# Kernel optimization log

Measured on AMD Instinct MI355X. Metric: run time of the kernel, lower is better.

Reference implementation:

```python
import jax, jax.numpy as jnp
import numpy as np

BLOCK_SIZE = 256
EMB = 384
HEAD = 64
B = 256
T = 256

def setup_inputs() -> dict:
    key = jax.random.key(0)
    k1, k2, k3, k4 = jax.random.split(key, 4)
    x = jax.random.normal(k1, (B, T, EMB), dtype=jnp.float32)
    # torch Linear(no bias) default init ~ U(-1/sqrt(in), 1/sqrt(in)); use scaled normal
    s = 1.0 / np.sqrt(EMB)
    Wq = jax.random.normal(k2, (EMB, HEAD), dtype=jnp.float32) * s
    Wk = jax.random.normal(k3, (EMB, HEAD), dtype=jnp.float32) * s
    Wv = jax.random.normal(k4, (EMB, HEAD), dtype=jnp.float32) * s
    return {"x": x, "Wq": Wq, "Wk": Wk, "Wv": Wv}

def reference(x, Wq, Wk, Wv):
    Bb, Tt, C = x.shape
    q = jnp.einsum('btc,ch->bth', x, Wq)
    k = jnp.einsum('btc,ch->bth', x, Wk)
    v = jnp.einsum('btc,ch->bth', x, Wv)
    # NOTE: source scales by C**-0.5 where C = embedding dim (384), not head_size
    scores = jnp.einsum('bth,bsh->bts', q, k) * (C ** -0.5)  # [B,T,T]
    causal = jnp.tril(jnp.ones((Tt, Tt), dtype=bool))
    scores = jnp.where(causal, scores, -jnp.inf)
    weights = jax.nn.softmax(scores, axis=-1)
    # dropout is identity in eval mode (reference baseline)
    out = jnp.einsum('bts,bsh->bth', weights, v)
    return out
```

## Files before the change

kernel.cpp:

```cpp
#include <hip/hip_runtime.h>
#include <hip/hip_bf16.h>
#include <cstdint>
#include <cstddef>

#define B_DIM 256
#define T_DIM 256
#define EMB   384
#define HEAD  64

typedef __attribute__((ext_vector_type(8))) short bf16x8;
typedef __attribute__((ext_vector_type(4))) float f32x4;
typedef __attribute__((ext_vector_type(4))) unsigned int u32x4;

__device__ __forceinline__ unsigned short f2bf(float f) {
    union { float f; unsigned int u; } v; v.f = f;
    unsigned int r = v.u + 0x7fffu + ((v.u >> 16) & 1u);
    return (unsigned short)(r >> 16);
}

__device__ __forceinline__ unsigned int pkbf(float a, float b) {
#if __has_builtin(__builtin_amdgcn_cvt_pk_bf16_f32)
    typedef __attribute__((ext_vector_type(2))) __bf16 bf16x2_t;
    bf16x2_t r = __builtin_amdgcn_cvt_pk_bf16_f32(a, b);
    return *(unsigned int*)&r;
#else
    return (unsigned)f2bf(a) | ((unsigned)f2bf(b) << 16);
#endif
}

__global__ void wprep_kernel(const float* __restrict__ Wq, const float* __restrict__ Wk,
                             const float* __restrict__ Wv, unsigned short* __restrict__ Wb) {
    int g = blockIdx.x * blockDim.x + threadIdx.x;
    if (g >= 9216) return;
    int kkstep = g / 1536, rem = g - kkstep * 1536;
    int r = rem >> 3, cs = rem & 7, c = cs ^ (r & 7);
    const float* W = (r < 64) ? Wq : (r < 128) ? Wk : Wv;
    int h = r & 63;
    unsigned short tmp[8];
#pragma unroll
    for (int e = 0; e < 8; ++e) {
        int k = kkstep * 64 + c * 8 + e;
        tmp[e] = f2bf(W[k * HEAD + h]);
    }
    *(u32x4*)(Wb + (size_t)g * 8) = *(u32x4*)tmp;
}

__global__ __launch_bounds__(512, 1) void fused_kernel(const float* __restrict__ x,
                                                       const unsigned short* __restrict__ Wb,
                                                       float* __restrict__ out) {
    __shared__ union SM {
        struct { unsigned short Xst[6][128][64]; unsigned short Ws[2][12288]; } p1;
        struct { unsigned short qs[256][72]; unsigned short ks[256][72];
                 unsigned short vT[64][264]; unsigned short Ps[8][16][72]; } p2;
    } sm;

    const int tid = threadIdx.x;
    const int w = tid >> 6, lane = tid & 63, qd = lane >> 4, l15 = lane & 15;
    const int wm = w >> 2, wn = w & 3;
    const int b = blockIdx.x;
    const float* xb = x + (size_t)b * T_DIM * EMB;
    const int trow = tid >> 4, fc = tid & 15;

#define WGLDS(KSTEP, BUF) do { \
    _Pragma("unroll") \
    for (int s = 0; s < 3; ++s) { \
        int idx = s * 512 + w * 64; \
        const unsigned short* gp = Wb + (size_t)((KSTEP) * 1536 + idx + lane) * 8; \
        unsigned short* lp = &sm.p1.Ws[BUF][idx * 8]; \
        __builtin_amdgcn_global_load_lds( \
            (const __attribute__((address_space(1))) unsigned int*)gp, \
            (__attribute__((address_space(3))) unsigned int*)lp, 16, 0, 0); \
    } \
} while (0)

#define XLOAD(P, RG) do { \
    _Pragma("unroll") \
    for (int kk = 0; kk < 6; ++kk) \
        xq[(RG) & 1][kk] = *(const float4*)(xb + (size_t)((P) * 128 + (RG) * 32 + trow) * EMB + kk * 64 + 4 * fc); \
} while (0)

#define XCW(RG) do { \
    int row_ = (RG) * 32 + trow; \
    _Pragma("unroll") \
    for (int kk = 0; kk < 6; ++kk) { \
        float4 v_ = xq[(RG) & 1][kk]; \
        *(uint2*)((char*)&sm.p1.Xst[kk][row_][0] + ((((fc >> 1) ^ (row_ & 7)) << 4) | ((fc & 1) << 3))) = \
            make_uint2(pkbf(v_.x, v_.y), pkbf(v_.z, v_.w)); \
    } \
} while (0)

    f32x4 acc[2][4][3];
#pragma unroll
    for (int P = 0; P < 2; ++P)
#pragma unroll
        for (int mt = 0; mt < 4; ++mt)
#pragma unroll
            for (int nt = 0; nt < 3; ++nt) acc[P][mt][nt] = (f32x4){0.f, 0.f, 0.f, 0.f};

    float4 xq[2][6];

#pragma unroll
    for (int P = 0; P < 2; ++P) {
        WGLDS(0, 0);
        XLOAD(P, 0); XLOAD(P, 1);
        XCW(0);
        XLOAD(P, 2);
        XCW(1);
        XLOAD(P, 3);
        XCW(2);
        XCW(3);

#pragma unroll
        for (int kk = 0; kk < 6; ++kk) {
            __syncthreads();
            if (kk < 5) WGLDS(kk + 1, (kk + 1) & 1);
#pragma unroll
            for (int kb = 0; kb < 2; ++kb) {
                bf16x8 a[4], bb[3];
#pragma unroll
                for (int mt = 0; mt < 4; ++mt) {
                    int rl = 64 * wm + 16 * mt + l15;
                    a[mt] = *(const bf16x8*)((const char*)&sm.p1.Xst[kk][rl][0] +
                                             ((((kb << 2) + qd) ^ (rl & 7)) << 4));
                }
#pragma unroll
                for (int nt = 0; nt < 3; ++nt) {
                    int n = 48 * wn + 16 * nt + l15;
                    bb[nt] = *(const bf16x8*)&sm.p1.Ws[kk & 1][n * 64 + (((4 * kb + qd) ^ (n & 7)) << 3)];
                }
#pragma unroll
                for (int mt = 0; mt < 4; ++mt)
#pragma unroll
                    for (int nt = 0; nt < 3; ++nt)
                        acc[P][mt][nt] = __builtin_amdgcn_mfma_f32_16x16x32_bf16(a[mt], bb[nt], acc[P][mt][nt], 0, 0, 0);
            }
        }
        __syncthreads();
    }

#pragma unroll
    for (int P = 0; P < 2; ++P)
#pragma unroll
        for (int nt = 0; nt < 3; ++nt) {
            int n = 48 * wn + 16 * nt + l15;
            int arr = n >> 6, hh = n & 63;
            if (arr == 2) {
#pragma unroll
                for (int mt = 0; mt < 4; ++mt) {
                    int tok0 = 128 * P + 64 * wm + 16 * mt + 4 * qd;
                    *(uint2*)&sm.p2.vT[hh][tok0] = make_uint2(
                        pkbf(acc[P][mt][nt][0], acc[P][mt][nt][1]),
                        pkbf(acc[P][mt][nt][2], acc[P][mt][nt][3]));
                }
            } else {
#pragma unroll
                for (int mt = 0; mt < 4; ++mt)
#pragma unroll
                    for (int reg = 0; reg < 4; ++reg) {
                        int tok = 128 * P + 64 * wm + 16 * mt + 4 * qd + reg;
                        unsigned short val = f2bf(acc[P][mt][nt][reg]);
                        if (arr == 0) sm.p2.qs[tok][hh] = val;
                        else          sm.p2.ks[tok][hh] = val;
                    }
            }
        }
    __syncthreads();

    const int tiles[2] = { w, 15 - w };
    bf16x8 aq[2][2];
#pragma unroll
    for (int ti = 0; ti < 2; ++ti)
#pragma unroll
        for (int kbi = 0; kbi < 2; ++kbi)
            aq[ti][kbi] = *(const bf16x8*)&sm.p2.qs[16 * tiles[ti] + l15][32 * kbi + 8 * qd];

    f32x4 O[2][4];
    float l[2][4];
#pragma unroll
    for (int ti = 0; ti < 2; ++ti) {
#pragma unroll
        for (int dn = 0; dn < 4; ++dn) O[ti][dn] = (f32x4){0.f, 0.f, 0.f, 0.f};
#pragma unroll
        for (int reg = 0; reg < 4; ++reg) l[ti][reg] = 0.f;
    }

    const float cExp = 1.4426950408889634f / 19.595917942265423f;

#pragma unroll
    for (int ti = 0; ti < 2; ++ti) {
        const int t = tiles[ti];
        for (int jc = 0; jc <= (t >> 2); ++jc) {
            const int ntmax = min(3, t - 4 * jc);
            f32x4 S[4];
#pragma unroll
            for (int nt = 0; nt < 4; ++nt) {
                if (nt <= ntmax) {
                    bf16x8 b0 = *(const bf16x8*)&sm.p2.ks[64 * jc + 16 * nt + l15][8 * qd];
                    bf16x8 b1 = *(const bf16x8*)&sm.p2.ks[64 * jc + 16 * nt + l15][32 + 8 * qd];
                    f32x4 s = __builtin_amdgcn_mfma_f32_16x16x32_bf16(aq[ti][0], b0, (f32x4){0.f,0.f,0.f,0.f}, 0, 0, 0);
                    s = __builtin_amdgcn_mfma_f32_16x16x32_bf16(aq[ti][1], b1, s, 0, 0, 0);
                    S[nt] = s;
                }
            }
#pragma unroll
            for (int nt = 0; nt < 4; ++nt) {
#pragma unroll
                for (int reg = 0; reg < 4; ++reg) {
                    float p = 0.0f;
                    if (nt <= ntmax) {
                        p = exp2f(S[nt][reg] * cExp);
                        if (4 * jc + nt == t && (l15 > 4 * qd + reg)) p = 0.0f;
                    }
                    l[ti][reg] += p;
                    sm.p2.Ps[w][4 * qd + reg][16 * nt + l15] = f2bf(p);
                }
            }
            bf16x8 ap0 = *(const bf16x8*)&sm.p2.Ps[w][l15][8 * qd];
            bf16x8 ap1 = *(const bf16x8*)&sm.p2.Ps[w][l15][32 + 8 * qd];
#pragma unroll
            for (int dn = 0; dn < 4; ++dn) {
                bf16x8 bv0 = *(const bf16x8*)&sm.p2.vT[16 * dn + l15][64 * jc + 8 * qd];
                bf16x8 bv1 = *(const bf16x8*)&sm.p2.vT[16 * dn + l15][64 * jc + 32 + 8 * qd];
                O[ti][dn] = __builtin_amdgcn_mfma_f32_16x16x32_bf16(ap0, bv0, O[ti][dn], 0, 0, 0);
                O[ti][dn] = __builtin_amdgcn_mfma_f32_16x16x32_bf16(ap1, bv1, O[ti][dn], 0, 0, 0);
            }
        }
    }

#pragma unroll
    for (int ti = 0; ti < 2; ++ti) {
#pragma unroll
        for (int reg = 0; reg < 4; ++reg) {
            float s = l[ti][reg];
            s += __shfl_xor(s, 1);
            s += __shfl_xor(s, 2);
            s += __shfl_xor(s, 4);
            s += __shfl_xor(s, 8);
            float inv = 1.0f / s;
            int row = 16 * tiles[ti] + 4 * qd + reg;
            float* dst = out + ((size_t)b * T_DIM + row) * HEAD;
#pragma unroll
            for (int dn = 0; dn < 4; ++dn)
                dst[16 * dn + l15] = O[ti][dn][reg] * inv;
        }
    }
}

extern "C" void kernel_launch(void* const* d_in, const int* in_sizes, int n_in,
                              void* d_out, int out_size, void* d_ws, size_t ws_size,
                              hipStream_t stream) {
    const float* x  = (const float*)d_in[0];
    const float* Wq = (const float*)d_in[1];
    const float* Wk = (const float*)d_in[2];
    const float* Wv = (const float*)d_in[3];
    float* out = (float*)d_out;

    unsigned short* Wb = (unsigned short*)d_ws;

    wprep_kernel<<<36, 256, 0, stream>>>(Wq, Wk, Wv, Wb);
    fused_kernel<<<B_DIM, 512, 0, stream>>>(x, Wb, out);
}
```

Baseline: 173.8 us.

## Double block to 1024 threads and stream x per k-step with double buffering

Raises the workgroup from 8 to 16 waves. The projection now covers all 256 tokens in one pass, with x loaded per 64-wide k-chunk into a double-buffered padded LDS tile and prefetched in registers across the MFMA loop. In the attention phase each wave owns one query tile instead of two, with tiles assigned so that long and short causal rows are spread across waves. This aims to raise latency hiding and parallelism per CU. In exchange, register budget per thread shrinks, there are more barriers per k-step, and the padded unswizzled x layout may cause LDS bank conflicts.

```diff
diff --git a/kernel.cpp b/kernel.cpp
--- a/kernel.cpp
+++ b/kernel.cpp
@@ -45,13 +45,13 @@
     *(u32x4*)(Wb + (size_t)g * 8) = *(u32x4*)tmp;
 }
 
-__global__ __launch_bounds__(512, 1) void fused_kernel(const float* __restrict__ x,
-                                                       const unsigned short* __restrict__ Wb,
-                                                       float* __restrict__ out) {
+__global__ __launch_bounds__(1024, 1) void fused_kernel(const float* __restrict__ x,
+                                                        const unsigned short* __restrict__ Wb,
+                                                        float* __restrict__ out) {
     __shared__ union SM {
-        struct { unsigned short Xst[6][128][64]; unsigned short Ws[2][12288]; } p1;
+        struct { unsigned short Xs[2][256][72]; unsigned short Ws[2][12288]; } p1;
         struct { unsigned short qs[256][72]; unsigned short ks[256][72];
-                 unsigned short vT[64][264]; unsigned short Ps[8][16][72]; } p2;
+                 unsigned short vT[64][264]; unsigned short Ps[16][16][72]; } p2;
     } sm;
 
     const int tid = threadIdx.x;
@@ -59,190 +59,167 @@
     const int wm = w >> 2, wn = w & 3;
     const int b = blockIdx.x;
     const float* xb = x + (size_t)b * T_DIM * EMB;
-    const int trow = tid >> 4, fc = tid & 15;
+    const int xrow = tid >> 2, xj = tid & 3;
 
 #define WGLDS(KSTEP, BUF) do { \
     _Pragma("unroll") \
-    for (int s = 0; s < 3; ++s) { \
-        int idx = s * 512 + w * 64; \
-        const unsigned short* gp = Wb + (size_t)((KSTEP) * 1536 + idx + lane) * 8; \
-        unsigned short* lp = &sm.p1.Ws[BUF][idx * 8]; \
-        __builtin_amdgcn_global_load_lds( \
-            (const __attribute__((address_space(1))) unsigned int*)gp, \
-            (__attribute__((address_space(3))) unsigned int*)lp, 16, 0, 0); \
+    for (int s = 0; s < 2; ++s) { \
+        int idx = s * 1024 + w * 64; \
+        if (idx < 1536) { \
+            const unsigned short* gp = Wb + (size_t)((KSTEP) * 1536 + idx + lane) * 8; \
+            unsigned short* lp = &sm.p1.Ws[BUF][idx * 8]; \
+            __builtin_amdgcn_global_load_lds( \
+                (const __attribute__((address_space(1))) unsigned int*)gp, \
+                (__attribute__((address_space(3))) unsigned int*)lp, 16, 0, 0); \
+        } \
     } \
 } while (0)
 
-#define XLOAD(P, RG) do { \
+#define XLOAD(KK) do { \
     _Pragma("unroll") \
-    for (int kk = 0; kk < 6; ++kk) \
-        xq[(RG) & 1][kk] = *(const float4*)(xb + (size_t)((P) * 128 + (RG) * 32 + trow) * EMB + kk * 64 + 4 * fc); \
+    for (int i = 0; i < 4; ++i) \
+        xr[i] = *(const float4*)(xb + (size_t)xrow * EMB + (KK) * 64 + (4 * xj + i) * 4); \
 } while (0)
 
-#define XCW(RG) do { \
-    int row_ = (RG) * 32 + trow; \
+#define XWRITE(BUF) do { \
     _Pragma("unroll") \
-    for (int kk = 0; kk < 6; ++kk) { \
-        float4 v_ = xq[(RG) & 1][kk]; \
-        *(uint2*)((char*)&sm.p1.Xst[kk][row_][0] + ((((fc >> 1) ^ (row_ & 7)) << 4) | ((fc & 1) << 3))) = \
-            make_uint2(pkbf(v_.x, v_.y), pkbf(v_.z, v_.w)); \
-    } \
+    for (int i = 0; i < 4; ++i) \
+        *(uint2*)&sm.p1.Xs[BUF][xrow][4 * (4 * xj + i)] = \
+            make_uint2(pkbf(xr[i].x, xr[i].y), pkbf(xr[i].z, xr[i].w)); \
 } while (0)
 
-    f32x4 acc[2][4][3];
-#pragma unroll
-    for (int P = 0; P < 2; ++P)
-#pragma unroll
-        for (int mt = 0; mt < 4; ++mt)
-#pragma unroll
-            for (int nt = 0; nt < 3; ++nt) acc[P][mt][nt] = (f32x4){0.f, 0.f, 0.f, 0.f};
-
-    float4 xq[2][6];
-
-#pragma unroll
-    for (int P = 0; P < 2; ++P) {
-        WGLDS(0, 0);
-        XLOAD(P, 0); XLOAD(P, 1);
-        XCW(0);
-        XLOAD(P, 2);
-        XCW(1);
-        XLOAD(P, 3);
-        XCW(2);
-        XCW(3);
-
-#pragma unroll
-        for (int kk = 0; kk < 6; ++kk) {
-            __syncthreads();
-            if (kk < 5) WGLDS(kk + 1, (kk + 1) & 1);
-#pragma unroll
-            for (int kb = 0; kb < 2; ++kb) {
-                bf16x8 a[4], bb[3];
-#pragma unroll
-                for (int mt = 0; mt < 4; ++mt) {
-                    int rl = 64 * wm + 16 * mt + l15;
-                    a[mt] = *(const bf16x8*)((const char*)&sm.p1.Xst[kk][rl][0] +
-                                             ((((kb << 2) + qd) ^ (rl & 7)) << 4));
+    float4 xr[4];
+    WGLDS(0, 0);
+    XLOAD(0);
+    XWRITE(0);
+
+    f32x4 acc[4][3];
+#pragma unroll
+    for (int mt = 0; mt < 4; ++mt)
+#pragma unroll
+        for (int nt = 0; nt < 3; ++nt) acc[mt][nt] = (f32x4){0.f, 0.f, 0.f, 0.f};
+
+#pragma unroll
+    for (int kk = 0; kk < 6; ++kk) {
+        __syncthreads();
+        if (kk < 5) {
+            WGLDS(kk + 1, (kk + 1) & 1);
+            XLOAD(kk + 1);
+        }
+#pragma unroll
+        for (int kb = 0; kb < 2; ++kb) {
+            bf16x8 a[4], bb[3];
+#pragma unroll
+            for (int mt = 0; mt < 4; ++mt)
+                a[mt] = *(const bf16x8*)&sm.p1.Xs[kk & 1][64 * wm + 16 * mt + l15][32 * kb + 8 * qd];
+#pragma unroll
+            for (int nt = 0; nt < 3; ++nt) {
+                int n = 48 * wn + 16 * nt + l15;
+                bb[nt] = *(const bf16x8*)&sm.p1.Ws[kk & 1][n * 64 + (((4 * kb + qd) ^ (n & 7)) << 3)];
+            }
+#pragma unroll
+            for (int mt = 0; mt < 4; ++mt)
+#pragma unroll
+                for (int nt = 0; nt < 3; ++nt)
+                    acc[mt][nt] = __builtin_amdgcn_mfma_f32_16x16x32_bf16(a[mt], bb[nt], acc[mt][nt], 0, 0, 0);
+        }
+        if (kk < 5) XWRITE((kk + 1) & 1);
+    }
+    __syncthreads();
+
+#pragma unroll
+    for (int nt = 0; nt < 3; ++nt) {
+        int n = 48 * wn + 16 * nt + l15;
+        int arr = n >> 6, hh = n & 63;
+        if (arr == 2) {
+#pragma unroll
+            for (int mt = 0; mt < 4; ++mt) {
+                int tok0 = 64 * wm + 16 * mt + 4 * qd;
+                *(uint2*)&sm.p2.vT[hh][tok0] = make_uint2(
+                    pkbf(acc[mt][nt][0], acc[mt][nt][1]),
+                    pkbf(acc[mt][nt][2], acc[mt][nt][3]));
+            }
+        } else {
+#pragma unroll
+            for (int mt = 0; mt < 4; ++mt)
+#pragma unroll
+                for (int reg = 0; reg < 4; ++reg) {
+                    int tok = 64 * wm + 16 * mt + 4 * qd + reg;
+                    unsigned short val = f2bf(acc[mt][nt][reg]);
+                    if (arr == 0) sm.p2.qs[tok][hh] = val;
+                    else          sm.p2.ks[tok][hh] = val;
                 }
-#pragma unroll
-                for (int nt = 0; nt < 3; ++nt) {
-                    int n = 48 * wn + 16 * nt + l15;
-                    bb[nt] = *(const bf16x8*)&sm.p1.Ws[kk & 1][n * 64 + (((4 * kb + qd) ^ (n & 7)) << 3)];
+        }
+    }
+    __syncthreads();
+
+    const int slot = w >> 2, sid = w & 3;
+    const int t = (slot < 2) ? (2 * sid + slot) : (15 - 2 * sid - (slot & 1));
+
+    bf16x8 aq[2];
+#pragma unroll
+    for (int kbi = 0; kbi < 2; ++kbi)
+        aq[kbi] = *(const bf16x8*)&sm.p2.qs[16 * t + l15][32 * kbi + 8 * qd];
+
+    f32x4 O[4];
+    float l[4];
+#pragma unroll
+    for (int dn = 0; dn < 4; ++dn) O[dn] = (f32x4){0.f, 0.f, 0.f, 0.f};
+#pragma unroll
+    for (int reg = 0; reg < 4; ++reg) l[reg] = 0.f;
+
+    const float cExp = 1.4426950408889634f / 19.595917942265423f;
+
+    for (int jc = 0; jc <= (t >> 2); ++jc) {
+        const int ntmax = min(3, t - 4 * jc);
+        f32x4 S[4];
+#pragma unroll
+        for (int nt = 0; nt < 4; ++nt) {
+            if (nt <= ntmax) {
+                bf16x8 b0 = *(const bf16x8*)&sm.p2.ks[64 * jc + 16 * nt + l15][8 * qd];
+                bf16x8 b1 = *(const bf16x8*)&sm.p2.ks[64 * jc + 16 * nt + l15][32 + 8 * qd];
+                f32x4 s = __builtin_amdgcn_mfma_f32_16x16x32_bf16(aq[0], b0, (f32x4){0.f,0.f,0.f,0.f}, 0, 0, 0);
+                s = __builtin_amdgcn_mfma_f32_16x16x32_bf16(aq[1], b1, s, 0, 0, 0);
+                S[nt] = s;
+            }
+        }
+#pragma unroll
+        for (int nt = 0; nt < 4; ++nt) {
+#pragma unroll
+            for (int reg = 0; reg < 4; ++reg) {
+                float p = 0.0f;
+                if (nt <= ntmax) {
+                    p = exp2f(S[nt][reg] * cExp);
+                    if (4 * jc + nt == t && (l15 > 4 * qd + reg)) p = 0.0f;
                 }
-#pragma unroll
-                for (int mt = 0; mt < 4; ++mt)
-#pragma unroll
-                    for (int nt = 0; nt < 3; ++nt)
-                        acc[P][mt][nt] = __builtin_amdgcn_mfma_f32_16x16x32_bf16(a[mt], bb[nt], acc[P][mt][nt], 0, 0, 0);
-            }
-        }
-        __syncthreads();
-    }
-
-#pragma unroll
-    for (int P = 0; P < 2; ++P)
-#pragma unroll
-        for (int nt = 0; nt < 3; ++nt) {
-            int n = 48 * wn + 16 * nt + l15;
-            int arr = n >> 6, hh = n & 63;
-            if (arr == 2) {
-#pragma unroll
-                for (int mt = 0; mt < 4; ++mt) {
-                    int tok0 = 128 * P + 64 * wm + 16 * mt + 4 * qd;
-                    *(uint2*)&sm.p2.vT[hh][tok0] = make_uint2(
-                        pkbf(acc[P][mt][nt][0], acc[P][mt][nt][1]),
-                        pkbf(acc[P][mt][nt][2], acc[P][mt][nt][3]));
-                }
-            } else {
-#pragma unroll
-                for (int mt = 0; mt < 4; ++mt)
-#pragma unroll
-                    for (int reg = 0; reg < 4; ++reg) {
-                        int tok = 128 * P + 64 * wm + 16 * mt + 4 * qd + reg;
-                        unsigned short val = f2bf(acc[P][mt][nt][reg]);
-                        if (arr == 0) sm.p2.qs[tok][hh] = val;
-                        else          sm.p2.ks[tok][hh] = val;
-                    }
-            }
-        }
-    __syncthreads();
-
-    const int tiles[2] = { w, 15 - w };
-    bf16x8 aq[2][2];
-#pragma unroll
-    for (int ti = 0; ti < 2; ++ti)
-#pragma unroll
-        for (int kbi = 0; kbi < 2; ++kbi)
-            aq[ti][kbi] = *(const bf16x8*)&sm.p2.qs[16 * tiles[ti] + l15][32 * kbi + 8 * qd];
-
-    f32x4 O[2][4];
-    float l[2][4];
-#pragma unroll
-    for (int ti = 0; ti < 2; ++ti) {
-#pragma unroll
-        for (int dn = 0; dn < 4; ++dn) O[ti][dn] = (f32x4){0.f, 0.f, 0.f, 0.f};
-#pragma unroll
-        for (int reg = 0; reg < 4; ++reg) l[ti][reg] = 0.f;
-    }
-
-    const float cExp = 1.4426950408889634f / 19.595917942265423f;
-
-#pragma unroll
-    for (int ti = 0; ti < 2; ++ti) {
-        const int t = tiles[ti];
-        for (int jc = 0; jc <= (t >> 2); ++jc) {
-            const int ntmax = min(3, t - 4 * jc);
-            f32x4 S[4];
-#pragma unroll
-            for (int nt = 0; nt < 4; ++nt) {
-                if (nt <= ntmax) {
-                    bf16x8 b0 = *(const bf16x8*)&sm.p2.ks[64 * jc + 16 * nt + l15][8 * qd];
-                    bf16x8 b1 = *(const bf16x8*)&sm.p2.ks[64 * jc + 16 * nt + l15][32 + 8 * qd];
-                    f32x4 s = __builtin_amdgcn_mfma_f32_16x16x32_bf16(aq[ti][0], b0, (f32x4){0.f,0.f,0.f,0.f}, 0, 0, 0);
-                    s = __builtin_amdgcn_mfma_f32_16x16x32_bf16(aq[ti][1], b1, s, 0, 0, 0);
-                    S[nt] = s;
-                }
-            }
-#pragma unroll
-            for (int nt = 0; nt < 4; ++nt) {
-#pragma unroll
-                for (int reg = 0; reg < 4; ++reg) {
-                    float p = 0.0f;
-                    if (nt <= ntmax) {
-                        p = exp2f(S[nt][reg] * cExp);
-                        if (4 * jc + nt == t && (l15 > 4 * qd + reg)) p = 0.0f;
-                    }
-                    l[ti][reg] += p;
-                    sm.p2.Ps[w][4 * qd + reg][16 * nt + l15] = f2bf(p);
-                }
-            }
-            bf16x8 ap0 = *(const bf16x8*)&sm.p2.Ps[w][l15][8 * qd];
-            bf16x8 ap1 = *(const bf16x8*)&sm.p2.Ps[w][l15][32 + 8 * qd];
-#pragma unroll
-            for (int dn = 0; dn < 4; ++dn) {
-                bf16x8 bv0 = *(const bf16x8*)&sm.p2.vT[16 * dn + l15][64 * jc + 8 * qd];
-                bf16x8 bv1 = *(const bf16x8*)&sm.p2.vT[16 * dn + l15][64 * jc + 32 + 8 * qd];
-                O[ti][dn] = __builtin_amdgcn_mfma_f32_16x16x32_bf16(ap0, bv0, O[ti][dn], 0, 0, 0);
-                O[ti][dn] = __builtin_amdgcn_mfma_f32_16x16x32_bf16(ap1, bv1, O[ti][dn], 0, 0, 0);
-            }
-        }
-    }
-
-#pragma unroll
-    for (int ti = 0; ti < 2; ++ti) {
-#pragma unroll
-        for (int reg = 0; reg < 4; ++reg) {
-            float s = l[ti][reg];
-            s += __shfl_xor(s, 1);
-            s += __shfl_xor(s, 2);
-            s += __shfl_xor(s, 4);
-            s += __shfl_xor(s, 8);
-            float inv = 1.0f / s;
-            int row = 16 * tiles[ti] + 4 * qd + reg;
-            float* dst = out + ((size_t)b * T_DIM + row) * HEAD;
-#pragma unroll
-            for (int dn = 0; dn < 4; ++dn)
-                dst[16 * dn + l15] = O[ti][dn][reg] * inv;
-        }
+                l[reg] += p;
+                sm.p2.Ps[w][4 * qd + reg][16 * nt + l15] = f2bf(p);
+            }
+        }
+        bf16x8 ap0 = *(const bf16x8*)&sm.p2.Ps[w][l15][8 * qd];
+        bf16x8 ap1 = *(const bf16x8*)&sm.p2.Ps[w][l15][32 + 8 * qd];
+#pragma unroll
+        for (int dn = 0; dn < 4; ++dn) {
+            bf16x8 bv0 = *(const bf16x8*)&sm.p2.vT[16 * dn + l15][64 * jc + 8 * qd];
+            bf16x8 bv1 = *(const bf16x8*)&sm.p2.vT[16 * dn + l15][64 * jc + 32 + 8 * qd];
+            O[dn] = __builtin_amdgcn_mfma_f32_16x16x32_bf16(ap0, bv0, O[dn], 0, 0, 0);
+            O[dn] = __builtin_amdgcn_mfma_f32_16x16x32_bf16(ap1, bv1, O[dn], 0, 0, 0);
+        }
+    }
+
+#pragma unroll
+    for (int reg = 0; reg < 4; ++reg) {
+        float s = l[reg];
+        s += __shfl_xor(s, 1);
+        s += __shfl_xor(s, 2);
+        s += __shfl_xor(s, 4);
+        s += __shfl_xor(s, 8);
+        float inv = 1.0f / s;
+        int row = 16 * t + 4 * qd + reg;
+        float* dst = out + ((size_t)b * T_DIM + row) * HEAD;
+#pragma unroll
+        for (int dn = 0; dn < 4; ++dn)
+            dst[16 * dn + l15] = O[dn][reg] * inv;
     }
 }
 
@@ -258,5 +235,5 @@
     unsigned short* Wb = (unsigned short*)d_ws;
 
     wprep_kernel<<<36, 256, 0, stream>>>(Wq, Wk, Wv, Wb);
-    fused_kernel<<<B_DIM, 512, 0, stream>>>(x, Wb, out);
-}
+    fused_kernel<<<B_DIM, 1024, 0, stream>>>(x, Wb, out);
+}
```

New measurement: 173.0 us. Within noise of the previous version (-0.4%).
